# Kernel tuning notes

Hardware: AMD Instinct MI355X
Metric: run time of the kernel (lower is better)

## Reference

```python
import jax, jax.numpy as jnp
import numpy as np

N, E, ET, C, H, L = 100000, 500000, 3, 128, 128, 3
LN_EPS = 1e-5
L2_EPS = 1e-12


def setup_inputs() -> dict:
    ks = jax.random.split(jax.random.key(0), 12)
    s = 0.05
    return {
        "x": jax.random.normal(ks[0], (N, C), jnp.float32),
        "edges": jax.random.randint(ks[1], (ET, 2, E), 0, N),
        "Wp": jax.random.normal(ks[2], (ET, C, C), jnp.float32) * s,
        "bp": jax.random.normal(ks[3], (ET, C), jnp.float32) * s,
        "Wl0": jax.random.normal(ks[4], (ET, C, H), jnp.float32) * s,
        "bl0": jax.random.normal(ks[5], (ET, H), jnp.float32) * s,
        "Wr0": jax.random.normal(ks[6], (ET, C, H), jnp.float32) * s,
        "Wl": jax.random.normal(ks[7], (L - 1, ET, H, H), jnp.float32) * s,
        "bl": jax.random.normal(ks[8], (L - 1, ET, H), jnp.float32) * s,
        "Wr": jax.random.normal(ks[9], (L - 1, ET, H, H), jnp.float32) * s,
        "ln_g": jnp.ones((L - 1, H), jnp.float32),
        "ln_b": jnp.zeros((L - 1, H), jnp.float32),
    }


def _mean_aggr(msg, dst, n):
    # scatter-mean of per-edge messages onto destination nodes
    summed = jax.ops.segment_sum(msg, dst, num_segments=n)
    deg = jax.ops.segment_sum(jnp.ones((dst.shape[0],), msg.dtype), dst, num_segments=n)
    return summed / jnp.maximum(deg, 1.0)[:, None]


def _sage(h, ei, Wl_, bl_, Wr_, Wp_=None, bp_=None, normalize=False):
    # PyG SAGEConv: out = lin_l(mean_{j in N(i)} h_j) + lin_r(h_i)
    src, dst = ei[0], ei[1]
    hs = jax.nn.relu(h @ Wp_ + bp_) if Wp_ is not None else h  # project=True path
    agg = _mean_aggr(hs[src], dst, h.shape[0])
    out = agg @ Wl_ + bl_ + h @ Wr_
    if normalize:
        out = out / jnp.maximum(jnp.linalg.norm(out, axis=-1, keepdims=True), L2_EPS)
    return out


def _layer_norm(h, g, b):
    mu = h.mean(-1, keepdims=True)
    var = ((h - mu) ** 2).mean(-1, keepdims=True)
    return (h - mu) / jnp.sqrt(var + LN_EPS) * g + b


def _forward(x, edges, Wp, bp, Wl0, bl0, Wr0, Wl, bl, Wr, ln_g, ln_b):
    et = edges.shape[0]
    # layer 0: project=True, normalize=True; HeteroConv mean over edge types
    h = sum(_sage(x, edges[t], Wl0[t], bl0[t], Wr0[t], Wp[t], bp[t], True)
            for t in range(et)) / et
    h = _layer_norm(jax.nn.relu(h), ln_g[0], ln_b[0])  # dropout = identity (eval)
    n_rest = Wl.shape[0]
    for l in range(n_rest):
        h = sum(_sage(h, edges[t], Wl[l, t], bl[l, t], Wr[l, t])
                for t in range(et)) / et
        if l != n_rest - 1:
            h = _layer_norm(jax.nn.relu(h), ln_g[l + 1], ln_b[l + 1])
    return h


def reference(x, edges, Wp, bp, Wl0, bl0, Wr0, Wl, bl, Wr, ln_g, ln_b):
    return _forward(x, edges, Wp, bp, Wl0, bl0, Wr0, Wl, bl, Wr, ln_g, ln_b)
```

## Files before the change

### kernel.cpp

```cpp
#include <hip/hip_runtime.h>
#include <math.h>

#define CH 128
#define ETC 3
#define LN_EPS 1e-5f
#define DEGCAP 32

typedef unsigned short u16;
typedef unsigned int u32;
typedef __attribute__((ext_vector_type(8))) short short8;
typedef __attribute__((ext_vector_type(4))) float f32x4;
typedef __attribute__((ext_vector_type(2))) float f32x2;

__device__ __forceinline__ u16 f2bf(float f) {
    u32 u = __float_as_uint(f);
    u += 0x7FFFu + ((u >> 16) & 1u);
    return (u16)(u >> 16);
}
__device__ __forceinline__ float bflo(u32 u) { return __uint_as_float(u << 16); }
__device__ __forceinline__ float bfhi(u32 u) { return __uint_as_float(u & 0xFFFF0000u); }

__device__ __forceinline__ f32x4 mfma16(short8 a, short8 b, f32x4 c) {
    return __builtin_amdgcn_mfma_f32_16x16x32_bf16(a, b, c, 0, 0, 0);
}
__device__ __forceinline__ short8 ld8(const u16* p) { return *(const short8*)p; }

__global__ __launch_bounds__(256) void pack_w(
    const float* __restrict__ Wp, const float* __restrict__ Wl0,
    const float* __restrict__ Wr0, const float* __restrict__ Wl,
    const float* __restrict__ Wr, const float* __restrict__ bl,
    u16* __restrict__ Bswz, float* __restrict__ bls)
{
    if (blockIdx.x == 0) {
        int l = threadIdx.x >> 7, i = threadIdx.x & 127;
        bls[threadIdx.x] = (bl[((size_t)l * ETC + 0) * CH + i] +
                            bl[((size_t)l * ETC + 1) * CH + i] +
                            bl[((size_t)l * ETC + 2) * CH + i]) * (1.f / 3.f);
    }
    int grp = blockIdx.x * 256 + threadIdx.x;
    if (grp >= 17 * 2048) return;
    int lane = grp & 63;
    int t1 = grp >> 6;
    int nt = t1 & 7, t2 = t1 >> 3;
    int s = t2 & 3, mat = t2 >> 2;
    int q = lane >> 4, c = lane & 15;
    int nn = nt * 16 + c;

    const float* s0;
    const float* s1 = nullptr;
    const float* s2 = nullptr;
    float scale = 1.f;
    if (mat < 3) {
        s0 = Wp + (size_t)mat * CH * CH;
    } else if (mat < 9) {
        int t = (mat - 3) >> 1;
        s0 = ((mat - 3) & 1) ? Wr0 + (size_t)t * CH * CH : Wl0 + (size_t)t * CH * CH;
    } else {
        int l = (mat < 13) ? 0 : 1;
        int mm = mat - (l ? 13 : 9);
        scale = 1.f / 3.f;
        if (mm < 3) s0 = Wl + ((size_t)l * ETC + mm) * CH * CH;
        else {
            s0 = Wr + ((size_t)l * ETC + 0) * CH * CH;
            s1 = s0 + CH * CH;
            s2 = s1 + CH * CH;
        }
    }
    short8 o;
    #pragma unroll
    for (int j = 0; j < 8; ++j) {
        int k = s * 32 + q * 8 + j;
        float v = s0[(size_t)k * CH + nn];
        if (s1) v += s1[(size_t)k * CH + nn] + s2[(size_t)k * CH + nn];
        o[j] = (short)f2bf(v * scale);
    }
    *(short8*)&Bswz[(size_t)grp * 8] = o;
}

__global__ __launch_bounds__(256) void cast_x(
    const float* __restrict__ x, u16* __restrict__ xb, int total)
{
    int i = (blockIdx.x * 256 + threadIdx.x) * 8;
    if (i >= total) return;
    short8 o;
    #pragma unroll
    for (int j = 0; j < 8; ++j) o[j] = (short)f2bf(x[i + j]);
    *(short8*)&xb[i] = o;
}

template<int MODE>
__global__ __launch_bounds__(256, MODE == 0 ? 3 : 4) void combine_k(
    const u16* __restrict__ agg0, const u16* __restrict__ agg1,
    const u16* __restrict__ agg2, const u16* __restrict__ self,
    const u16* __restrict__ Bs, const float* __restrict__ bias,
    const float* __restrict__ lg, const float* __restrict__ lb,
    u16* __restrict__ outb, float* __restrict__ outf, int nrows)
{
    __shared__ __align__(16) u16 Bsh[CH * CH];
    const int tid = threadIdx.x;
    const int w = tid >> 6, lane = tid & 63;
    const int q = lane >> 4, c = lane & 15;
    const int rbase = (blockIdx.x * 4 + w) * 16;
    const int arow = rbase + c;
    constexpr int NM = (MODE == 0) ? 6 : ((MODE == 3) ? 1 : 4);
    constexpr int NA = (MODE == 3) ? 1 : 4;

    const u16* As[4];
    if constexpr (MODE == 3) {
        As[0] = self;
    } else {
        As[0] = agg0; As[1] = agg1; As[2] = agg2; As[3] = self;
    }

    short8 af[NA][4];
    #pragma unroll
    for (int a = 0; a < NA; ++a)
        #pragma unroll
        for (int s = 0; s < 4; ++s)
            af[a][s] = ld8(&As[a][(size_t)arow * CH + s * 32 + q * 8]);

    f32x4 acc[8] = {};
    f32x4 res[8] = {};

    #pragma unroll
    for (int m = 0; m < NM; ++m) {
        __syncthreads();
        const u16* bsrc = Bs + (size_t)m * CH * CH;
        #pragma unroll
        for (int i = 0; i < 8; ++i)
            *(short8*)&Bsh[(i * 256 + tid) * 8] = ld8(&bsrc[(i * 256 + tid) * 8]);
        __syncthreads();

        constexpr int AI_TBL0[6] = {0, 3, 1, 3, 2, 3};
        const int ai = (MODE == 0) ? AI_TBL0[m]
                     : (MODE == 3) ? 0
                     : ((m < 3) ? m : 3);

        #pragma unroll
        for (int s = 0; s < 4; ++s) {
            #pragma unroll
            for (int nt = 0; nt < 8; ++nt) {
                short8 bv = *(const short8*)&Bsh[((size_t)(s * 8 + nt) * 64 + lane) * 8];
                acc[nt] = mfma16(af[ai][s], bv, acc[nt]);
            }
        }

        if constexpr (MODE == 0) {
            if (m & 1) {
                const int t = m >> 1;
                float ss[4] = {0.f, 0.f, 0.f, 0.f};
                #pragma unroll
                for (int nt = 0; nt < 8; ++nt) {
                    float bf = bias[t * CH + nt * 16 + c];
                    #pragma unroll
                    for (int r = 0; r < 4; ++r) {
                        float v = acc[nt][r] + bf;
                        acc[nt][r] = v;
                        ss[r] += v * v;
                    }
                }
                #pragma unroll
                for (int msk = 1; msk < 16; msk <<= 1)
                    #pragma unroll
                    for (int r = 0; r < 4; ++r) ss[r] += __shfl_xor(ss[r], msk, 64);
                float sc[4];
                #pragma unroll
                for (int r = 0; r < 4; ++r)
                    sc[r] = 1.f / (3.f * fmaxf(sqrtf(ss[r]), 1e-12f));
                #pragma unroll
                for (int nt = 0; nt < 8; ++nt)
                    #pragma unroll
                    for (int r = 0; r < 4; ++r) {
                        res[nt][r] += acc[nt][r] * sc[r];
                        acc[nt][r] = 0.f;
                    }
            }
        }
    }

    if constexpr (MODE != 0) {
        #pragma unroll
        for (int nt = 0; nt < 8; ++nt) {
            float bv = bias[nt * 16 + c];
            #pragma unroll
            for (int r = 0; r < 4; ++r) res[nt][r] = acc[nt][r] + bv;
        }
    }

    if constexpr (MODE == 2) {
        #pragma unroll
        for (int nt = 0; nt < 8; ++nt)
            #pragma unroll
            for (int r = 0; r < 4; ++r) {
                int row = rbase + q * 4 + r;
                if (row < nrows) outf[(size_t)row * CH + nt * 16 + c] = res[nt][r];
            }
        return;
    }

    if constexpr (MODE == 3) {
        #pragma unroll
        for (int nt = 0; nt < 8; ++nt)
            #pragma unroll
            for (int r = 0; r < 4; ++r) {
                int row = rbase + q * 4 + r;
                outb[(size_t)row * CH + nt * 16 + c] = f2bf(fmaxf(res[nt][r], 0.f));
            }
        return;
    }

    {
        float s1[4] = {0.f, 0.f, 0.f, 0.f}, s2[4] = {0.f, 0.f, 0.f, 0.f};
        #pragma unroll
        for (int nt = 0; nt < 8; ++nt)
            #pragma unroll
            for (int r = 0; r < 4; ++r) {
                float v = fmaxf(res[nt][r], 0.f);
                res[nt][r] = v;
                s1[r] += v;
                s2[r] += v * v;
            }
        #pragma unroll
        for (int msk = 1; msk < 16; msk <<= 1)
            #pragma unroll
            for (int r = 0; r < 4; ++r) {
                s1[r] += __shfl_xor(s1[r], msk, 64);
                s2[r] += __shfl_xor(s2[r], msk, 64);
            }
        float mu[4], rs[4];
        #pragma unroll
        for (int r = 0; r < 4; ++r) {
            mu[r] = s1[r] * (1.f / 128.f);
            float var = s2[r] * (1.f / 128.f) - mu[r] * mu[r];
            rs[r] = rsqrtf(var + LN_EPS);
        }
        #pragma unroll
        for (int nt = 0; nt < 8; ++nt) {
            float gv = lg[nt * 16 + c], bv = lb[nt * 16 + c];
            #pragma unroll
            for (int r = 0; r < 4; ++r) {
                int row = rbase + q * 4 + r;
                outb[(size_t)row * CH + nt * 16 + c] =
                    f2bf((res[nt][r] - mu[r]) * rs[r] * gv + bv);
            }
        }
    }
}

#define ACC4(v) do { \
        f32x2 aa, bb; \
        aa[0] = bflo((v).x); aa[1] = bflo((v).y); ev01 += aa; \
        bb[0] = bfhi((v).x); bb[1] = bfhi((v).y); od01 += bb; \
        aa[0] = bflo((v).z); aa[1] = bflo((v).w); ev23 += aa; \
        bb[0] = bfhi((v).z); bb[1] = bfhi((v).w); od23 += bb; \
    } while (0)

__global__ __launch_bounds__(256) void agg_k(
    const u16* __restrict__ msg, const int* __restrict__ cnt,
    const int* __restrict__ col, u16* __restrict__ agg, int n,
    int cntstride, unsigned long long colstride, unsigned long long aggstride)
{
    const int t = blockIdx.y;
    cnt += (size_t)t * cntstride;
    col += (size_t)t * colstride;
    agg += (size_t)t * aggstride;

    int gid = blockIdx.x * 256 + threadIdx.x;
    int node = gid >> 4;
    int lane = threadIdx.x & 15;
    if (node >= n) return;
    int deg = cnt[node];
    int e = min(deg, DEGCAP);
    const int* cl = col + (size_t)node * DEGCAP;
    const uint4* m128 = (const uint4*)msg;

    f32x2 ev01 = {0.f, 0.f}, ev23 = {0.f, 0.f};
    f32x2 od01 = {0.f, 0.f}, od23 = {0.f, 0.f};

    int j = 0;
    for (; j + 4 <= e; j += 4) {
        int c0 = cl[j], c1 = cl[j + 1], c2 = cl[j + 2], c3 = cl[j + 3];
        uint4 v0 = m128[(size_t)c0 * 16 + lane];
        uint4 v1 = m128[(size_t)c1 * 16 + lane];
        uint4 v2 = m128[(size_t)c2 * 16 + lane];
        uint4 v3 = m128[(size_t)c3 * 16 + lane];
        ACC4(v0); ACC4(v1); ACC4(v2); ACC4(v3);
    }
    for (; j < e; ++j) {
        uint4 v0 = m128[(size_t)cl[j] * 16 + lane];
        ACC4(v0);
    }
    float inv = 1.f / (float)max(deg, 1);
    uint4 o;
    o.x = (u32)f2bf(ev01[0] * inv) | ((u32)f2bf(od01[0] * inv) << 16);
    o.y = (u32)f2bf(ev01[1] * inv) | ((u32)f2bf(od01[1] * inv) << 16);
    o.z = (u32)f2bf(ev23[0] * inv) | ((u32)f2bf(od23[0] * inv) << 16);
    o.w = (u32)f2bf(ev23[1] * inv) | ((u32)f2bf(od23[1] * inv) << 16);
    ((uint4*)agg)[(size_t)node * 16 + lane] = o;
}

__global__ __launch_bounds__(256) void fillpad_k(
    const int* __restrict__ edges, int* __restrict__ cnt,
    int* __restrict__ colbuf, int E, int n, int npad)
{
    int t = blockIdx.y;
    int o = blockIdx.x & 7;
    int base = (blockIdx.x >> 3) * 2048 + threadIdx.x * 8;
    const int* srcp = edges + (size_t)t * 2 * E;
    const int* dstp = srcp + E;
    int* cntt = cnt + (size_t)t * n;
    int* colt = colbuf + (size_t)t * npad * DEGCAP;
#define PUT(dv, sv) \
    if ((((dv) >> 7) & 7) == o) { \
        int pos = atomicAdd(&cntt[dv], 1); \
        if (pos < DEGCAP) colt[(size_t)(dv) * DEGCAP + pos] = (sv); \
    }
    #pragma unroll
    for (int h = 0; h < 2; ++h) {
        int e = base + h * 4;
        if (e + 4 <= E) {
            int4 d = *(const int4*)&dstp[e];
            PUT(d.x, srcp[e]);
            PUT(d.y, srcp[e + 1]);
            PUT(d.z, srcp[e + 2]);
            PUT(d.w, srcp[e + 3]);
        } else {
            for (int k = 0; k < 4; ++k)
                if (e + k < E) { int dv = dstp[e + k]; PUT(dv, srcp[e + k]); }
        }
    }
#undef PUT
}

extern "C" void kernel_launch(void* const* d_in, const int* in_sizes, int n_in,
                              void* d_out, int out_size, void* d_ws, size_t ws_size,
                              hipStream_t stream) {
    const float* x    = (const float*)d_in[0];
    const int*   edges= (const int*)d_in[1];
    const float* Wp   = (const float*)d_in[2];
    const float* bp   = (const float*)d_in[3];
    const float* Wl0  = (const float*)d_in[4];
    const float* bl0  = (const float*)d_in[5];
    const float* Wr0  = (const float*)d_in[6];
    const float* Wl   = (const float*)d_in[7];
    const float* bl   = (const float*)d_in[8];
    const float* Wr   = (const float*)d_in[9];
    const float* ln_g = (const float*)d_in[10];
    const float* ln_b = (const float*)d_in[11];
    float* out = (float*)d_out;

    const int n  = in_sizes[0] / CH;
    const int E  = in_sizes[1] / (2 * ETC);
    const int npad = ((n + 255) / 256) * 256;
    const size_t MS = (size_t)CH * CH;

    char* p = (char*)d_ws;
    u16* xb   = (u16*)p;  p += (size_t)npad * CH * 2;
    u16* hs   = (u16*)p;  p += (size_t)npad * CH * 2;
    u16* agg  = (u16*)p;  p += (size_t)ETC * npad * CH * 2;
    u16* Bswz = (u16*)p;  p += 17 * MS * 2;
    float* bls = (float*)p; p += 256 * 4;
    int* cnt    = (int*)p;  p += (size_t)ETC * n * 4;
    int* colbuf = (int*)p;

    const dim3 b256(256);
    const dim3 ge8(((E + 2047) / 2048) * 8, ETC);
    const int gb = (n + 63) / 64;
    const int ga = (n * 16 + 255) / 256;
    const unsigned long long colstr = (unsigned long long)npad * DEGCAP;
    const unsigned long long aggstr = (unsigned long long)npad * CH;

    hipMemsetAsync(cnt, 0, (size_t)ETC * n * sizeof(int), stream);
    fillpad_k<<<ge8, b256, 0, stream>>>(edges, cnt, colbuf, E, n, npad);

    pack_w<<<136, b256, 0, stream>>>(Wp, Wl0, Wr0, Wl, Wr, bl, Bswz, bls);
    cast_x<<<(n * CH / 8 + 255) / 256, b256, 0, stream>>>(x, xb, n * CH);

    for (int t = 0; t < ETC; ++t) {
        combine_k<3><<<gb, b256, 0, stream>>>(
            nullptr, nullptr, nullptr, xb, Bswz + (size_t)t * MS, bp + t * CH,
            nullptr, nullptr, hs, nullptr, n);
        agg_k<<<dim3(ga, 1), b256, 0, stream>>>(hs, cnt + (size_t)t * n,
                                                colbuf + (size_t)t * colstr,
                                                agg + (size_t)t * aggstr, n,
                                                0, 0ull, 0ull);
    }
    combine_k<0><<<gb, b256, 0, stream>>>(agg, agg + aggstr, agg + 2 * aggstr, xb,
                                          Bswz + 3 * MS, bl0, ln_g, ln_b, hs, nullptr, n);

    agg_k<<<dim3(ga, ETC), b256, 0, stream>>>(hs, cnt, colbuf, agg, n,
                                              n, colstr, aggstr);
    combine_k<1><<<gb, b256, 0, stream>>>(agg, agg + aggstr, agg + 2 * aggstr, hs,
                                          Bswz + 9 * MS, bls, ln_g + CH, ln_b + CH,
                                          hs, nullptr, n);

    agg_k<<<dim3(ga, ETC), b256, 0, stream>>>(hs, cnt, colbuf, agg, n,
                                              n, colstr, aggstr);
    combine_k<2><<<gb, b256, 0, stream>>>(agg, agg + aggstr, agg + 2 * aggstr, hs,
                                          Bswz + 13 * MS, bls + CH, nullptr, nullptr,
                                          nullptr, out, n);
}
```

Before: 576.5 us.

## Fuse neighbor mean-aggregation into combine kernels and batch projections

Removes the separate agg_k launches. Each combine block now gathers and averages neighbor rows for its 64 nodes into shared memory, then feeds them directly to the MFMA matmuls. The three per-edge-type projections are merged into one proj3_k kernel that writes three buffers, and layer outputs ping-pong between hs and the reused projection buffer to avoid in-place hazards. This drops the agg buffer round-trip through global memory and several launches, but puts the latency-bound gather inside a kernel with heavier LDS use and lower occupancy.

```diff
diff --git a/kernel.cpp b/kernel.cpp
--- a/kernel.cpp
+++ b/kernel.cpp
@@ -88,13 +88,18 @@
     *(short8*)&xb[i] = o;
 }
 
-template<int MODE>
-__global__ __launch_bounds__(256, MODE == 0 ? 3 : 4) void combine_k(
-    const u16* __restrict__ agg0, const u16* __restrict__ agg1,
-    const u16* __restrict__ agg2, const u16* __restrict__ self,
-    const u16* __restrict__ Bs, const float* __restrict__ bias,
-    const float* __restrict__ lg, const float* __restrict__ lb,
-    u16* __restrict__ outb, float* __restrict__ outf, int nrows)
+#define ACC4(v) do { \
+        f32x2 aa, bb; \
+        aa[0] = bflo((v).x); aa[1] = bflo((v).y); ev01 += aa; \
+        bb[0] = bfhi((v).x); bb[1] = bfhi((v).y); od01 += bb; \
+        aa[0] = bflo((v).z); aa[1] = bflo((v).w); ev23 += aa; \
+        bb[0] = bfhi((v).z); bb[1] = bfhi((v).w); od23 += bb; \
+    } while (0)
+
+__global__ __launch_bounds__(256, 4) void proj3_k(
+    const u16* __restrict__ xb, const u16* __restrict__ Bs,
+    const float* __restrict__ bp,
+    u16* __restrict__ p0, u16* __restrict__ p1, u16* __restrict__ p2)
 {
     __shared__ __align__(16) u16 Bsh[CH * CH];
     const int tid = threadIdx.x;
@@ -102,22 +107,114 @@
     const int q = lane >> 4, c = lane & 15;
     const int rbase = (blockIdx.x * 4 + w) * 16;
     const int arow = rbase + c;
-    constexpr int NM = (MODE == 0) ? 6 : ((MODE == 3) ? 1 : 4);
-    constexpr int NA = (MODE == 3) ? 1 : 4;
-
-    const u16* As[4];
-    if constexpr (MODE == 3) {
-        As[0] = self;
-    } else {
-        As[0] = agg0; As[1] = agg1; As[2] = agg2; As[3] = self;
-    }
-
-    short8 af[NA][4];
-    #pragma unroll
-    for (int a = 0; a < NA; ++a)
+    u16* outs[3] = {p0, p1, p2};
+
+    short8 af[4];
+    #pragma unroll
+    for (int s = 0; s < 4; ++s)
+        af[s] = ld8(&xb[(size_t)arow * CH + s * 32 + q * 8]);
+
+    #pragma unroll
+    for (int m = 0; m < 3; ++m) {
+        __syncthreads();
+        const u16* bsrc = Bs + (size_t)m * CH * CH;
+        #pragma unroll
+        for (int i = 0; i < 8; ++i)
+            *(short8*)&Bsh[(i * 256 + tid) * 8] = ld8(&bsrc[(i * 256 + tid) * 8]);
+        __syncthreads();
+
+        f32x4 acc[8] = {};
         #pragma unroll
         for (int s = 0; s < 4; ++s)
-            af[a][s] = ld8(&As[a][(size_t)arow * CH + s * 32 + q * 8]);
+            #pragma unroll
+            for (int nt = 0; nt < 8; ++nt) {
+                short8 bv = *(const short8*)&Bsh[((size_t)(s * 8 + nt) * 64 + lane) * 8];
+                acc[nt] = mfma16(af[s], bv, acc[nt]);
+            }
+        u16* ob = outs[m];
+        #pragma unroll
+        for (int nt = 0; nt < 8; ++nt) {
+            float bv = bp[m * CH + nt * 16 + c];
+            #pragma unroll
+            for (int r = 0; r < 4; ++r) {
+                int row = rbase + q * 4 + r;
+                ob[(size_t)row * CH + nt * 16 + c] = f2bf(fmaxf(acc[nt][r] + bv, 0.f));
+            }
+        }
+    }
+}
+
+template<int MODE>
+__global__ __launch_bounds__(256, 3) void combine_k(
+    const u16* __restrict__ g0, const u16* __restrict__ g1,
+    const u16* __restrict__ g2, const u16* __restrict__ self,
+    const int* __restrict__ cnt, const int* __restrict__ colbuf,
+    int n, unsigned long long colstride,
+    const u16* __restrict__ Bs, const float* __restrict__ bias,
+    const float* __restrict__ lg, const float* __restrict__ lb,
+    u16* __restrict__ outb, float* __restrict__ outf)
+{
+    __shared__ __align__(16) u16 Bsh[CH * CH];
+    __shared__ __align__(16) uint4 Ash[64 * 17];
+    const int tid = threadIdx.x;
+    const int w = tid >> 6, lane = tid & 63;
+    const int q = lane >> 4, c = lane & 15;
+    const int rbase = (blockIdx.x * 4 + w) * 16;
+    const int arow = rbase + c;
+    constexpr int NM = (MODE == 0) ? 6 : 4;
+
+    const u16* gsrc[3] = {g0, g1, g2};
+
+    short8 af[4][4];
+    #pragma unroll
+    for (int s = 0; s < 4; ++s)
+        af[3][s] = ld8(&self[(size_t)arow * CH + s * 32 + q * 8]);
+
+    const int qw = tid >> 4, ql = tid & 15;
+    #pragma unroll
+    for (int t = 0; t < 3; ++t) {
+        if (t) __syncthreads();
+        const uint4* m128 = (const uint4*)gsrc[t];
+        const int* cntt = cnt + (size_t)t * n;
+        const int* colt = colbuf + (size_t)t * colstride;
+        #pragma unroll
+        for (int i = 0; i < 4; ++i) {
+            int ndl = qw * 4 + i;
+            int nd = blockIdx.x * 64 + ndl;
+            f32x2 ev01 = {0.f, 0.f}, ev23 = {0.f, 0.f};
+            f32x2 od01 = {0.f, 0.f}, od23 = {0.f, 0.f};
+            int deg = 0;
+            if (nd < n) {
+                deg = cntt[nd];
+                int e = min(deg, DEGCAP);
+                const int* cl = colt + (size_t)nd * DEGCAP;
+                int j = 0;
+                for (; j + 4 <= e; j += 4) {
+                    int c0 = cl[j], c1 = cl[j + 1], c2 = cl[j + 2], c3 = cl[j + 3];
+                    uint4 v0 = m128[(size_t)c0 * 16 + ql];
+                    uint4 v1 = m128[(size_t)c1 * 16 + ql];
+                    uint4 v2 = m128[(size_t)c2 * 16 + ql];
+                    uint4 v3 = m128[(size_t)c3 * 16 + ql];
+                    ACC4(v0); ACC4(v1); ACC4(v2); ACC4(v3);
+                }
+                for (; j < e; ++j) {
+                    uint4 v0 = m128[(size_t)cl[j] * 16 + ql];
+                    ACC4(v0);
+                }
+            }
+            float inv = 1.f / (float)max(deg, 1);
+            uint4 o;
+            o.x = (u32)f2bf(ev01[0] * inv) | ((u32)f2bf(od01[0] * inv) << 16);
+            o.y = (u32)f2bf(ev01[1] * inv) | ((u32)f2bf(od01[1] * inv) << 16);
+            o.z = (u32)f2bf(ev23[0] * inv) | ((u32)f2bf(od23[0] * inv) << 16);
+            o.w = (u32)f2bf(ev23[1] * inv) | ((u32)f2bf(od23[1] * inv) << 16);
+            Ash[(size_t)ndl * 17 + ql] = o;
+        }
+        __syncthreads();
+        #pragma unroll
+        for (int s = 0; s < 4; ++s)
+            af[t][s] = *(const short8*)&Ash[(size_t)(w * 16 + c) * 17 + s * 4 + q];
+    }
 
     f32x4 acc[8] = {};
     f32x4 res[8] = {};
@@ -132,9 +229,7 @@
         __syncthreads();
 
         constexpr int AI_TBL0[6] = {0, 3, 1, 3, 2, 3};
-        const int ai = (MODE == 0) ? AI_TBL0[m]
-                     : (MODE == 3) ? 0
-                     : ((m < 3) ? m : 3);
+        const int ai = (MODE == 0) ? AI_TBL0[m] : ((m < 3) ? m : 3);
 
         #pragma unroll
         for (int s = 0; s < 4; ++s) {
@@ -193,18 +288,7 @@
             #pragma unroll
             for (int r = 0; r < 4; ++r) {
                 int row = rbase + q * 4 + r;
-                if (row < nrows) outf[(size_t)row * CH + nt * 16 + c] = res[nt][r];
-            }
-        return;
-    }
-
-    if constexpr (MODE == 3) {
-        #pragma unroll
-        for (int nt = 0; nt < 8; ++nt)
-            #pragma unroll
-            for (int r = 0; r < 4; ++r) {
-                int row = rbase + q * 4 + r;
-                outb[(size_t)row * CH + nt * 16 + c] = f2bf(fmaxf(res[nt][r], 0.f));
+                if (row < n) outf[(size_t)row * CH + nt * 16 + c] = res[nt][r];
             }
         return;
     }
@@ -245,58 +329,6 @@
             }
         }
     }
-}
-
-#define ACC4(v) do { \
-        f32x2 aa, bb; \
-        aa[0] = bflo((v).x); aa[1] = bflo((v).y); ev01 += aa; \
-        bb[0] = bfhi((v).x); bb[1] = bfhi((v).y); od01 += bb; \
-        aa[0] = bflo((v).z); aa[1] = bflo((v).w); ev23 += aa; \
-        bb[0] = bfhi((v).z); bb[1] = bfhi((v).w); od23 += bb; \
-    } while (0)
-
-__global__ __launch_bounds__(256) void agg_k(
-    const u16* __restrict__ msg, const int* __restrict__ cnt,
-    const int* __restrict__ col, u16* __restrict__ agg, int n,
-    int cntstride, unsigned long long colstride, unsigned long long aggstride)
-{
-    const int t = blockIdx.y;
-    cnt += (size_t)t * cntstride;
-    col += (size_t)t * colstride;
-    agg += (size_t)t * aggstride;
-
-    int gid = blockIdx.x * 256 + threadIdx.x;
-    int node = gid >> 4;
-    int lane = threadIdx.x & 15;
-    if (node >= n) return;
-    int deg = cnt[node];
-    int e = min(deg, DEGCAP);
-    const int* cl = col + (size_t)node * DEGCAP;
-    const uint4* m128 = (const uint4*)msg;
-
-    f32x2 ev01 = {0.f, 0.f}, ev23 = {0.f, 0.f};
-    f32x2 od01 = {0.f, 0.f}, od23 = {0.f, 0.f};
-
-    int j = 0;
-    for (; j + 4 <= e; j += 4) {
-        int c0 = cl[j], c1 = cl[j + 1], c2 = cl[j + 2], c3 = cl[j + 3];
-        uint4 v0 = m128[(size_t)c0 * 16 + lane];
-        uint4 v1 = m128[(size_t)c1 * 16 + lane];
-        uint4 v2 = m128[(size_t)c2 * 16 + lane];
-        uint4 v3 = m128[(size_t)c3 * 16 + lane];
-        ACC4(v0); ACC4(v1); ACC4(v2); ACC4(v3);
-    }
-    for (; j < e; ++j) {
-        uint4 v0 = m128[(size_t)cl[j] * 16 + lane];
-        ACC4(v0);
-    }
-    float inv = 1.f / (float)max(deg, 1);
-    uint4 o;
-    o.x = (u32)f2bf(ev01[0] * inv) | ((u32)f2bf(od01[0] * inv) << 16);
-    o.y = (u32)f2bf(ev01[1] * inv) | ((u32)f2bf(od01[1] * inv) << 16);
-    o.z = (u32)f2bf(ev23[0] * inv) | ((u32)f2bf(od23[0] * inv) << 16);
-    o.w = (u32)f2bf(ev23[1] * inv) | ((u32)f2bf(od23[1] * inv) << 16);
-    ((uint4*)agg)[(size_t)node * 16 + lane] = o;
 }
 
 __global__ __launch_bounds__(256) void fillpad_k(
@@ -357,18 +389,19 @@
     char* p = (char*)d_ws;
     u16* xb   = (u16*)p;  p += (size_t)npad * CH * 2;
     u16* hs   = (u16*)p;  p += (size_t)npad * CH * 2;
-    u16* agg  = (u16*)p;  p += (size_t)ETC * npad * CH * 2;
+    u16* proj = (u16*)p;  p += (size_t)ETC * npad * CH * 2;
     u16* Bswz = (u16*)p;  p += 17 * MS * 2;
     float* bls = (float*)p; p += 256 * 4;
     int* cnt    = (int*)p;  p += (size_t)ETC * n * 4;
     int* colbuf = (int*)p;
 
+    const unsigned long long pstr = (unsigned long long)npad * CH;
+    u16* hs2 = proj;
+
     const dim3 b256(256);
     const dim3 ge8(((E + 2047) / 2048) * 8, ETC);
     const int gb = (n + 63) / 64;
-    const int ga = (n * 16 + 255) / 256;
     const unsigned long long colstr = (unsigned long long)npad * DEGCAP;
-    const unsigned long long aggstr = (unsigned long long)npad * CH;
 
     hipMemsetAsync(cnt, 0, (size_t)ETC * n * sizeof(int), stream);
     fillpad_k<<<ge8, b256, 0, stream>>>(edges, cnt, colbuf, E, n, npad);
@@ -376,27 +409,20 @@
     pack_w<<<136, b256, 0, stream>>>(Wp, Wl0, Wr0, Wl, Wr, bl, Bswz, bls);
     cast_x<<<(n * CH / 8 + 255) / 256, b256, 0, stream>>>(x, xb, n * CH);
 
-    for (int t = 0; t < ETC; ++t) {
-        combine_k<3><<<gb, b256, 0, stream>>>(
-            nullptr, nullptr, nullptr, xb, Bswz + (size_t)t * MS, bp + t * CH,
-            nullptr, nullptr, hs, nullptr, n);
-        agg_k<<<dim3(ga, 1), b256, 0, stream>>>(hs, cnt + (size_t)t * n,
-                                                colbuf + (size_t)t * colstr,
-                                                agg + (size_t)t * aggstr, n,
-                                                0, 0ull, 0ull);
-    }
-    combine_k<0><<<gb, b256, 0, stream>>>(agg, agg + aggstr, agg + 2 * aggstr, xb,
-                                          Bswz + 3 * MS, bl0, ln_g, ln_b, hs, nullptr, n);
-
-    agg_k<<<dim3(ga, ETC), b256, 0, stream>>>(hs, cnt, colbuf, agg, n,
-                                              n, colstr, aggstr);
-    combine_k<1><<<gb, b256, 0, stream>>>(agg, agg + aggstr, agg + 2 * aggstr, hs,
+    proj3_k<<<gb, b256, 0, stream>>>(xb, Bswz, bp,
+                                     proj, proj + pstr, proj + 2 * pstr);
+    combine_k<0><<<gb, b256, 0, stream>>>(proj, proj + pstr, proj + 2 * pstr, xb,
+                                          cnt, colbuf, n, colstr,
+                                          Bswz + 3 * MS, bl0, ln_g, ln_b,
+                                          hs, nullptr);
+
+    combine_k<1><<<gb, b256, 0, stream>>>(hs, hs, hs, hs,
+                                          cnt, colbuf, n, colstr,
                                           Bswz + 9 * MS, bls, ln_g + CH, ln_b + CH,
-                                          hs, nullptr, n);
-
-    agg_k<<<dim3(ga, ETC), b256, 0, stream>>>(hs, cnt, colbuf, agg, n,
-                                              n, colstr, aggstr);
-    combine_k<2><<<gb, b256, 0, stream>>>(agg, agg + aggstr, agg + 2 * aggstr, hs,
+                                          hs2, nullptr);
+
+    combine_k<2><<<gb, b256, 0, stream>>>(hs2, hs2, hs2, hs2,
+                                          cnt, colbuf, n, colstr,
                                           Bswz + 13 * MS, bls + CH, nullptr, nullptr,
-                                          nullptr, out, n);
-}
+                                          nullptr, out);
+}
```

New measurement: 701.1 us. +21.6%, slower.
